# Kernel tuning notes

Measured on AMD Instinct MI355X. Metric: run time of the kernel, lower is better.

## Reference

```python
import jax, jax.numpy as jnp
import numpy as np

MAX_LENGTH = 400
NULL_TERM_IND = 52
THR = 1.0 - 1e-05  # F.threshold threshold value


def leaky(x):
    # F.leaky_relu default negative_slope=0.01
    return jnp.where(x >= 0, x, 0.01 * x)


def gru_cell(x, h, w_ih, w_hh, b_ih, b_hh):
    # torch.nn.GRUCell math
    gi = x @ w_ih.T + b_ih          # [B, 3H]
    gh = h @ w_hh.T + b_hh          # [B, 3H]
    i_r, i_z, i_n = jnp.split(gi, 3, axis=-1)
    h_r, h_z, h_n = jnp.split(gh, 3, axis=-1)
    r = jax.nn.sigmoid(i_r + h_r)
    z = jax.nn.sigmoid(i_z + h_z)
    n = jnp.tanh(i_n + r * h_n)
    return (1.0 - z) * n + z * h


def setup_inputs() -> dict:
    key = jax.random.key(0)
    ks = jax.random.split(key, 9)
    B, D, H, C = 2048, 4096, 128, 96
    def init(k, shape, fan):
        return (jax.random.uniform(k, shape, jnp.float32) * 2.0 - 1.0) / np.sqrt(fan)
    return {
        "img_feat": jax.random.normal(ks[0], (B, D), jnp.float32),
        "lin1_w": init(ks[1], (H, D), D),
        "lin1_b": init(ks[2], (H,), D),
        "w_ih": init(ks[3], (3 * H, H), H),
        "w_hh": init(ks[4], (3 * H, H), H),
        "b_ih": init(ks[5], (3 * H,), H),
        "b_hh": init(ks[6], (3 * H,), H),
        "lin2_w": init(ks[7], (C, H), H),
        "lin2_b": init(ks[8], (C,), H),
    }


def reference(img_feat, lin1_w, lin1_b, w_ih, w_hh, b_ih, b_hh, lin2_w, lin2_b):
    # ht: GRU input at t=0 is leaky_relu(lin1(img_feat)); hidden starts at zeros.
    ht = leaky(img_feat @ lin1_w.T + lin1_b)   # [B, 128]
    h0 = jnp.zeros_like(ht)

    def step(carry, _):
        ht, h0 = carry
        hn = gru_cell(ht, h0, w_ih, w_hh, b_ih, b_hh)
        # original: ht = char_gen(ht, h0); h0 = ht -> input == hidden next step
        chars = leaky(hn) @ lin2_w.T + lin2_b   # [B, C]
        m = jax.lax.stop_gradient(jnp.max(chars, axis=-1, keepdims=True))  # .data detach
        cn = chars / m
        cn = jnp.where(cn > THR, cn, 0.0)       # F.threshold(x, 1-1e-5, 0)
        return (hn, hn), cn

    _, titles = jax.lax.scan(step, (ht, h0), None, length=MAX_LENGTH)  # [T, B, C]
    titles = jnp.transpose(titles, (1, 0, 2))   # [B, T, C]

    # title_lens: first t with titles[b, t, NULL_TERM_IND] == 1, else MAX_LENGTH
    eq = titles[:, :, NULL_TERM_IND] == 1.0     # [B, T]
    first = jnp.argmax(eq, axis=1)
    lens = jnp.where(eq.any(axis=1), first + 1, MAX_LENGTH).astype(jnp.int32)
    return titles, lens
```

## Files before the change

kernel.cpp:

```cpp
#include <hip/hip_runtime.h>
#include <math.h>

#define NB   8
#define TT   400
#define HH   128
#define CC   96
#define DD   4096
#define THRV (1.0f - 1e-5f)
#define XR   40
#define HEPS 4e-6f
#define S10  1024.0f
#define IS10 0.0009765625f
#define IS20 9.5367431640625e-07f

typedef _Float16 f16x8 __attribute__((ext_vector_type(8)));
typedef float    f32x4 __attribute__((ext_vector_type(4)));
typedef float    f32x2 __attribute__((ext_vector_type(2)));
typedef int      i32x4 __attribute__((ext_vector_type(4)));
typedef unsigned long long ull;

__device__ __forceinline__ float rcp_fast(float x) {
#if __has_builtin(__builtin_amdgcn_rcpf)
    return __builtin_amdgcn_rcpf(x);
#else
    return 1.0f / x;
#endif
}
__device__ __forceinline__ float sigm(float v)  { return rcp_fast(1.0f + __expf(-v)); }
__device__ __forceinline__ float ftanh(float x) { return 1.0f - 2.0f * rcp_fast(1.0f + __expf(2.0f * x)); }

__device__ __forceinline__ void split2(float4 u0, float4 u1, f16x8& hi, f16x8& lo) {
    float x[8] = {u0.x, u0.y, u0.z, u0.w, u1.x, u1.y, u1.z, u1.w};
    #pragma unroll
    for (int e = 0; e < 8; ++e) {
        _Float16 h = (_Float16)x[e];
        hi[e] = h;
        lo[e] = (_Float16)(x[e] - (float)h);
    }
}
__device__ __forceinline__ void split2s(float4 u0, float4 u1, f16x8& hi, f16x8& lo) {
    float x[8] = {u0.x, u0.y, u0.z, u0.w, u1.x, u1.y, u1.z, u1.w};
    #pragma unroll
    for (int e = 0; e < 8; ++e) {
        _Float16 h = (_Float16)x[e];
        hi[e] = h;
        lo[e] = (_Float16)((x[e] - (float)h) * S10);
    }
}
__device__ __forceinline__ void split1(float x, _Float16& hi, _Float16& lo) {
    hi = (_Float16)x;
    lo = (_Float16)(x - (float)hi);
}

__device__ __forceinline__ float xsum32(float v) {
#if __has_builtin(__builtin_amdgcn_permlane32_swap)
    auto r = __builtin_amdgcn_permlane32_swap(__float_as_uint(v), __float_as_uint(v), false, false);
    return __uint_as_float(r[0]) + __uint_as_float(r[1]);
#else
    return v + __shfl_xor(v, 32, 64);
#endif
}

__device__ __forceinline__ void step_barrier() {
    __builtin_amdgcn_sched_barrier(0);
    asm volatile("s_waitcnt lgkmcnt(0)" ::: "memory");
    __builtin_amdgcn_s_barrier();
    asm volatile("" ::: "memory");
    __builtin_amdgcn_sched_barrier(0);
}

__global__ __launch_bounds__(1024, 4)
void gru_title(const float* __restrict__ img,
               const float* __restrict__ l1w,
               const float* __restrict__ l1b,
               const float* __restrict__ wih,
               const float* __restrict__ whh,
               const float* __restrict__ bih,
               const float* __restrict__ bhh,
               const float* __restrict__ l2w,
               const float* __restrict__ l2b,
               float* __restrict__ out,
               float* __restrict__ lens)
{
    __shared__ alignas(16) _Float16 x2 [2][64][XR];
    __shared__ alignas(16) _Float16 l2v[2][64][XR];
    __shared__ alignas(16) char     x2i8[2][64][32];
    __shared__ alignas(16) _Float16 bcS[2][6][4][4][16][8];
    __shared__ alignas(16) float    gEx[4096];
    __shared__ alignas(16) float    scr[2048];
    __shared__ alignas(16) float    xs0[NB][HH];
    __shared__ int sh_st[4];

    const int tid  = threadIdx.x;
    const int b0   = blockIdx.x * NB;
    const int w    = tid >> 6;
    const int lane = tid & 63;
    const int lm   = lane & 15;
    const int lq   = lane >> 4;
    const int c8   = w & 7;
    const int r8   = w >> 3;
    const int ic2  = 16 * c8 + lm;

    f16x8 bh[2][4];
    i32x4 bq[2][2];
    float gb[2], fq[2];
    #pragma unroll
    for (int gl = 0; gl < 2; ++gl) {
        const int g2 = 2 * r8 + gl;
        const float* r0;
        const float* r1 = nullptr;
        float bsum;
        if (g2 == 0)      { r0 = wih + (size_t)ic2 * HH;         r1 = whh + (size_t)ic2 * HH;         bsum = bih[ic2] + bhh[ic2]; }
        else if (g2 == 1) { r0 = wih + (size_t)(128 + ic2) * HH; r1 = whh + (size_t)(128 + ic2) * HH; bsum = bih[128 + ic2] + bhh[128 + ic2]; }
        else if (g2 == 2) { r0 = wih + (size_t)(256 + ic2) * HH;                                      bsum = bih[256 + ic2]; }
        else              { r0 = whh + (size_t)(256 + ic2) * HH;                                      bsum = bhh[256 + ic2]; }
        gb[gl] = bsum;
        float bl32[4][8];
        #pragma unroll
        for (int kt = 0; kt < 4; ++kt) {
            const int k0 = 32 * kt + 8 * lq;
            float4 u0 = *(const float4*)(r0 + k0);
            float4 u1 = *(const float4*)(r0 + k0 + 4);
            if (r1) {
                float4 e0 = *(const float4*)(r1 + k0);
                float4 e1 = *(const float4*)(r1 + k0 + 4);
                u0.x += e0.x; u0.y += e0.y; u0.z += e0.z; u0.w += e0.w;
                u1.x += e1.x; u1.y += e1.y; u1.z += e1.z; u1.w += e1.w;
            }
            float xv[8] = {u0.x, u0.y, u0.z, u0.w, u1.x, u1.y, u1.z, u1.w};
            f16x8 hiv;
            #pragma unroll
            for (int e = 0; e < 8; ++e) {
                _Float16 hh = (_Float16)xv[e];
                hiv[e] = hh;
                bl32[kt][e] = xv[e] - (float)hh;
            }
            bh[gl][kt] = hiv;
        }
        float mx = 0.f;
        #pragma unroll
        for (int kt = 0; kt < 4; ++kt)
            #pragma unroll
            for (int e = 0; e < 8; ++e) mx = fmaxf(mx, fabsf(bl32[kt][e]));
        mx = fmaxf(mx, __shfl_xor(mx, 16, 64));
        mx = fmaxf(mx, __shfl_xor(mx, 32, 64));
        const float inv = (mx > 0.f) ? 127.0f / mx : 0.f;
        fq[gl] = mx * (1.0f / 16129.0f);
        ull p[4];
        #pragma unroll
        for (int kt = 0; kt < 4; ++kt) {
            ull pv = 0;
            #pragma unroll
            for (int e = 0; e < 8; ++e) {
                int q = (int)rintf(bl32[kt][e] * inv);
                pv |= ((ull)((unsigned)q & 0xffu)) << (8 * e);
            }
            p[kt] = pv;
        }
        #pragma unroll
        for (int ktp = 0; ktp < 2; ++ktp) {
            ull s0a = __shfl(p[2 * ktp],     lm + 16 * ((2 * lq) & 3), 64);
            ull s0b = __shfl(p[2 * ktp + 1], lm + 16 * ((2 * lq) & 3), 64);
            ull lo8 = (lq & 2) ? s0b : s0a;
            ull s1a = __shfl(p[2 * ktp],     lm + 16 * ((2 * lq + 1) & 3), 64);
            ull s1b = __shfl(p[2 * ktp + 1], lm + 16 * ((2 * lq + 1) & 3), 64);
            ull hi8 = (lq & 2) ? s1b : s1a;
            i32x4 f;
            f[0] = (int)(unsigned)(lo8 & 0xffffffffu);
            f[1] = (int)(unsigned)(lo8 >> 32);
            f[2] = (int)(unsigned)(hi8 & 0xffffffffu);
            f[3] = (int)(unsigned)(hi8 >> 32);
            bq[gl][ktp] = f;
        }
    }

    const int ct = (w >= 1 && w <= 6) ? (w - 1) : -1;
    float cb = 0.f;
    if (ct >= 0) cb = l2b[16 * ct + lm];

    for (int idx = tid; idx < 6 * 4 * 4 * 16; idx += 1024) {
        int t_  = idx;
        int lm_ = t_ & 15; t_ >>= 4;
        int lq_ = t_ & 3;  t_ >>= 2;
        int kt_ = t_ & 3;  t_ >>= 2;
        int ct_ = t_;
        const int n  = 16 * ct_ + lm_;
        const int k0 = 32 * kt_ + 8 * lq_;
        #pragma unroll
        for (int e = 0; e < 8; ++e) {
            float v = l2w[(size_t)n * HH + k0 + e];
            _Float16 hi = (_Float16)v;
            bcS[0][ct_][kt_][lq_][lm_][e] = hi;
            bcS[1][ct_][kt_][lq_][lm_][e] = (_Float16)(v - (float)hi);
        }
    }

    if (tid < 4) sh_st[tid] = 1;
    ((int*)x2i8)[tid] = 0;

    {
        const int m8 = lm & 7;
        const float* arow = img + (size_t)(b0 + m8) * DD + 8 * lq + 2048 * r8;
        const float* brow = l1w + (size_t)ic2 * DD + 8 * lq + 2048 * r8;
        f32x4 z4 = {0.f, 0.f, 0.f, 0.f};
        f32x4 accP0 = z4, accP1 = z4, accQ0 = z4, accQ1 = z4;
        auto ptile = [&](int kt, f32x4& aP, f32x4& aQ) {
            float4 a0  = *(const float4*)(arow + 32 * kt);
            float4 a1  = *(const float4*)(arow + 32 * kt + 4);
            float4 bb0 = *(const float4*)(brow + 32 * kt);
            float4 bb1 = *(const float4*)(brow + 32 * kt + 4);
            f16x8 ah, al, bhf, blf;
            split2s(a0, a1, ah, al);
            split2s(bb0, bb1, bhf, blf);
            f16x8 af = (lm >= 8) ? al : ah;
            aP = __builtin_amdgcn_mfma_f32_16x16x32_f16(af, bhf, aP, 0, 0, 0);
            aQ = __builtin_amdgcn_mfma_f32_16x16x32_f16(af, blf, aQ, 0, 0, 0);
        };
        #pragma unroll 2
        for (int kt = 0; kt < 64; kt += 2) {
            ptile(kt,     accP0, accQ0);
            ptile(kt + 1, accP1, accQ1);
        }
        f32x4 P = accP0 + accP1;
        f32x4 Q = accQ0 + accQ1;
        const float sP = (lane < 32) ? 1.0f : IS10;
        const float sQ = (lane < 32) ? IS10 : IS20;
        float s0 = xsum32(P[0] * sP + Q[0] * sQ);
        float s1 = xsum32(P[1] * sP + Q[1] * sQ);
        float s2 = xsum32(P[2] * sP + Q[2] * sQ);
        float s3 = xsum32(P[3] * sP + Q[3] * sQ);
        if (lane < 32) {
            float vv[4] = {s0, s1, s2, s3};
            #pragma unroll
            for (int reg = 0; reg < 4; ++reg)
                scr[r8 * 1024 + (4 * lq + reg) * 128 + ic2] = vv[reg];
        }
    }
    __syncthreads();
    {
        const int m = tid >> 7, c = tid & 127;
        float v = scr[m * 128 + c] + scr[1024 + m * 128 + c] + l1b[c];
        xs0[m][c] = (v >= 0.f) ? v : 0.01f * v;
    }
    __syncthreads();

    const int mA = (lane < 32) ? 4 * lq : 4 * (lq - 2) + 2;

    const int mB  = w >> 1;
    const int iB  = 64 * (w & 1) + lane;
    const int rBq = 16 * ((iB >> 3) & 3);
    const int cBq = 8 * (iB >> 5) + (iB & 7);
    const int r8q = 16 * ((iB >> 4) & 3) + mB;
    const int c8q = 16 * (iB >> 6) + (iB & 15);
    const unsigned gRd = (unsigned)(mB * 2048 + iB * 16) ^ ((unsigned)(mB & 3) << 5);

    float hreg = 0.f;
    int  len   = TT;
    bool found = false;
    int  tex   = TT;

    auto chars_mfma = [&](int slot, f32x4& cA, f32x4& cB) {
        #pragma unroll
        for (int kt = 0; kt < 4; ++kt) {
            f16x8 cf = *(const f16x8*)&l2v[slot][lane][8 * kt];
            f16x8 bH = *(const f16x8*)&bcS[0][ct][kt][lq][lm][0];
            f16x8 bL = *(const f16x8*)&bcS[1][ct][kt][lq][lm][0];
            f32x4& a = (kt < 2) ? cA : cB;
            a = __builtin_amdgcn_mfma_f32_16x16x32_f16(cf, bH, a, 0, 0, 0);
            a = __builtin_amdgcn_mfma_f32_16x16x32_f16(cf, bL, a, 0, 0, 0);
        }
    };
    auto chars_commit = [&](int slot, f32x4 cA, f32x4 cB) {
        f32x4 ca = cA + cB;
        const int n = 16 * ct + lm;
        float s0 = xsum32(ca[0]);
        float s1 = xsum32(ca[1]);
        float s2 = xsum32(ca[2]);
        float s3 = xsum32(ca[3]);
        scr[slot * 1024 + mA * 128 + n]       = ((lane < 32) ? s0 : s2) + cb;
        scr[slot * 1024 + (mA + 1) * 128 + n] = ((lane < 32) ? s1 : s3) + cb;
    };

    auto outrow = [&](int slot, int tme, int r) {
        const float* cr = &scr[slot * 1024 + r * 128];
        float a0 = cr[lane];
        float a1 = cr[32 + lane];
        float a2 = cr[64 + lane];
        float mx = fmaxf(fmaxf(a0, a1), a2);
        mx = fmaxf(mx, __shfl_xor(mx, 16, 32));
        mx = fmaxf(mx, __shfl_xor(mx, 8, 32));
        mx = fmaxf(mx, __shfl_xor(mx, 4, 32));
        mx = fmaxf(mx, __shfl_xor(mx, 2, 32));
        mx = fmaxf(mx, __shfl_xor(mx, 1, 32));
        float q0 = a0 / mx;
        float q1 = a1 / mx;
        float q2 = a2 / mx;
        if (lane < 32) {
            size_t base = ((size_t)(b0 + r) * TT + tme) * CC;
            out[base + lane]      = (q0 > THRV) ? q0 : 0.f;
            out[base + 32 + lane] = (q1 > THRV) ? q1 : 0.f;
            out[base + 64 + lane] = (q2 > THRV) ? q2 : 0.f;
        }
        float q52 = __shfl(q1, 20, 64);
        if (!found && q52 == 1.0f) { found = true; len = tme + 1; }
    };

    for (int t = 0; t < TT; ++t) {
        const int pr = (t + 1) & 1;
        const int pc = t & 1;

        if (t == 0) {
            if (tid < 512) {
                const int g = tid >> 7;
                const int i = tid & 127;
                float bsum;
                if (g == 0)      bsum = bih[i] + bhh[i];
                else if (g == 1) bsum = bih[128 + i] + bhh[128 + i];
                else if (g == 2) bsum = bih[256 + i];
                else             bsum = bhh[256 + i];
                float accT[NB];
                #pragma unroll
                for (int m = 0; m < NB; ++m) accT[m] = bsum;
                if (g < 3) {
                    const float4* wp = (const float4*)(wih + (size_t)(128 * g + i) * HH);
                    #pragma unroll
                    for (int k = 0; k < HH / 4; ++k) {
                        float4 wv = wp[k];
                        #pragma unroll
                        for (int m = 0; m < NB; ++m) {
                            float4 x = *(const float4*)&xs0[m][4 * k];
                            accT[m] += wv.x * x.x + wv.y * x.y + wv.z * x.z + wv.w * x.w;
                        }
                    }
                }
                #pragma unroll
                for (int m = 0; m < NB; ++m) {
                    unsigned off = (unsigned)(m * 2048 + i * 16 + g * 4) ^ ((unsigned)(m & 3) << 5);
                    *(float*)((char*)gEx + off) = accT[m];
                }
            }
        } else {
            f32x4 z4 = {0.f, 0.f, 0.f, 0.f};
            i32x4 iz = {0, 0, 0, 0};
            if (ct >= 0) {
                f32x4 cc0 = z4, cc1 = z4;
                chars_mfma(pr, cc0, cc1);
                chars_commit(pr, cc0, cc1);
            }
            f32x4 acc[2] = {z4, z4};
            i32x4 qac[2] = {iz, iz};
            {
                f16x8 afA = *(const f16x8*)&x2[pr][lane][0];
                f16x8 afB = *(const f16x8*)&x2[pr][lane][8];
                acc[0] = __builtin_amdgcn_mfma_f32_16x16x32_f16(afA, bh[0][0], acc[0], 0, 0, 0);
                acc[1] = __builtin_amdgcn_mfma_f32_16x16x32_f16(afA, bh[1][0], acc[1], 0, 0, 0);
                acc[0] = __builtin_amdgcn_mfma_f32_16x16x32_f16(afB, bh[0][1], acc[0], 0, 0, 0);
                acc[1] = __builtin_amdgcn_mfma_f32_16x16x32_f16(afB, bh[1][1], acc[1], 0, 0, 0);
                afA = *(const f16x8*)&x2[pr][lane][16];
                afB = *(const f16x8*)&x2[pr][lane][24];
                acc[0] = __builtin_amdgcn_mfma_f32_16x16x32_f16(afA, bh[0][2], acc[0], 0, 0, 0);
                acc[1] = __builtin_amdgcn_mfma_f32_16x16x32_f16(afA, bh[1][2], acc[1], 0, 0, 0);
                acc[0] = __builtin_amdgcn_mfma_f32_16x16x32_f16(afB, bh[0][3], acc[0], 0, 0, 0);
                acc[1] = __builtin_amdgcn_mfma_f32_16x16x32_f16(afB, bh[1][3], acc[1], 0, 0, 0);
                i32x4 ia = *(const i32x4*)&x2i8[pr][lane][0];
                qac[0] = __builtin_amdgcn_mfma_i32_16x16x64_i8(ia, bq[0][0], qac[0], 0, 0, 0);
                qac[1] = __builtin_amdgcn_mfma_i32_16x16x64_i8(ia, bq[1][0], qac[1], 0, 0, 0);
                ia = *(const i32x4*)&x2i8[pr][lane][16];
                qac[0] = __builtin_amdgcn_mfma_i32_16x16x64_i8(ia, bq[0][1], qac[0], 0, 0, 0);
                qac[1] = __builtin_amdgcn_mfma_i32_16x16x64_i8(ia, bq[1][1], qac[1], 0, 0, 0);
            }
            float G[2][2];
            #pragma unroll
            for (int gl = 0; gl < 2; ++gl) {
                f32x4 t4;
                #pragma unroll
                for (int rr = 0; rr < 4; ++rr)
                    t4[rr] = acc[gl][rr] + fq[gl] * (float)qac[gl][rr];
                float c0 = xsum32(t4[0]);
                float c1 = xsum32(t4[1]);
                float c2 = xsum32(t4[2]);
                float c3 = xsum32(t4[3]);
                G[gl][0] = ((lane < 32) ? c0 : c2) + gb[gl];
                G[gl][1] = ((lane < 32) ? c1 : c3) + gb[gl];
            }
            #pragma unroll
            for (int s = 0; s < 2; ++s) {
                const int m = mA + s;
                unsigned off = (unsigned)(m * 2048 + ic2 * 16 + r8 * 8) ^ ((unsigned)(m & 3) << 5);
                f32x2 v2 = {G[0][s], G[1][s]};
                *(f32x2*)((char*)gEx + off) = v2;
            }
        }
        step_barrier();

        {
            float4 g4 = *(const float4*)((const char*)gEx + gRd);
            float r = sigm(g4.x);
            float z = sigm(g4.y);
            float n = ftanh(g4.z + r * g4.w);
            float hp = (t == 0) ? 0.f : hreg;
            float h  = (1.f - z) * n + z * hp;
            bool chg = (t < 2) | (fabsf(h - hp) > HEPS);
            hreg = h;
            float lv = (h >= 0.f) ? h : 0.01f * h;
            _Float16 a, b;
            split1(h, a, b);
            x2[pc][rBq + mB][cBq]     = a;
            x2[pc][rBq + 8 + mB][cBq] = b;
            split1(lv, a, b);
            l2v[pc][rBq + mB][cBq]     = a;
            l2v[pc][rBq + 8 + mB][cBq] = b;
            x2i8[pc][r8q][c8q] = (char)(int)rintf(h * 127.0f);
            if (chg) sh_st[t & 3] = 0;
        }
        if (w >= 8 && t >= 2) outrow(pc, t - 2, w - 8);
        if (tid == 0) sh_st[(t + 2) & 3] = 1;
        step_barrier();
        if (t >= 2 && sh_st[t & 3]) { tex = t; break; }
    }

    if (tex == TT) {
        const int pl = (TT - 1) & 1;
        if (ct >= 0) {
            f32x4 z4 = {0.f, 0.f, 0.f, 0.f};
            f32x4 cc0 = z4, cc1 = z4;
            chars_mfma(pl, cc0, cc1);
            chars_commit(pl, cc0, cc1);
        }
        if (w >= 8) outrow(TT & 1, TT - 2, w - 8);
        __syncthreads();
        if (w >= 8) outrow(pl, TT - 1, w - 8);
    } else if (w >= 8) {
        const int r = w - 8;
        outrow((tex + 1) & 1, tex - 1, r);
        size_t rowbase = (size_t)(b0 + r) * TT * CC;
        #pragma unroll
        for (int p = 0; p < 2; ++p) {
            const float* cr = &scr[p * 1024 + r * 128];
            float a0 = cr[lane];
            float a1 = cr[32 + lane];
            float a2 = cr[64 + lane];
            float mx = fmaxf(fmaxf(a0, a1), a2);
            mx = fmaxf(mx, __shfl_xor(mx, 16, 32));
            mx = fmaxf(mx, __shfl_xor(mx, 8, 32));
            mx = fmaxf(mx, __shfl_xor(mx, 4, 32));
            mx = fmaxf(mx, __shfl_xor(mx, 2, 32));
            mx = fmaxf(mx, __shfl_xor(mx, 1, 32));
            const int u0 = tex + (((tex & 1) == p) ? 0 : 1);
            if (lane < 32) {
                float q0 = a0 / mx;
                float q1 = a1 / mx;
                float q2 = a2 / mx;
                float w0v = (q0 > THRV) ? q0 : 0.f;
                float w1v = (q1 > THRV) ? q1 : 0.f;
                float w2v = (q2 > THRV) ? q2 : 0.f;
                for (int u = u0; u < TT; u += 2) {
                    out[rowbase + (size_t)u * CC + lane]      = w0v;
                    out[rowbase + (size_t)u * CC + 32 + lane] = w1v;
                    out[rowbase + (size_t)u * CC + 64 + lane] = w2v;
                }
            }
        }
    }

    if (w >= 8 && lane == 0) lens[b0 + (w - 8)] = (float)len;
}

extern "C" void kernel_launch(void* const* d_in, const int* in_sizes, int n_in,
                              void* d_out, int out_size, void* d_ws, size_t ws_size,
                              hipStream_t stream)
{
    const float* img = (const float*)d_in[0];
    const float* l1w = (const float*)d_in[1];
    const float* l1b = (const float*)d_in[2];
    const float* wih = (const float*)d_in[3];
    const float* whh = (const float*)d_in[4];
    const float* bih = (const float*)d_in[5];
    const float* bhh = (const float*)d_in[6];
    const float* l2w = (const float*)d_in[7];
    const float* l2b = (const float*)d_in[8];

    float* out  = (float*)d_out;
    float* lens = out + (size_t)2048 * TT * CC;

    gru_title<<<dim3(2048 / NB), dim3(1024), 0, stream>>>(
        img, l1w, l1b, wih, whh, bih, bhh, l2w, l2b, out, lens);
}
```

Measured before the change: 581.2 us.

## Pad and XOR-swizzle shared buffers, move output row write before step barrier

Pads the scratch rows from 128 to 132 floats and XOR-swizzles the column-block index of the x2/l2v fp16 fragments by quarter-lane group, so MFMA operand loads and hidden-state stores hit different LDS banks. It also moves the per-row output normalisation and store (outrow) from after the GRU update into the else-branch before the first step barrier, so it overlaps with gate-computing waves. The intent is to cut LDS bank conflicts and shorten the serial per-step critical path. The risk is a read-after-write race on the scr slot that outrow now reads in a different phase of the step.

```diff
diff --git a/kernel.cpp b/kernel.cpp
--- a/kernel.cpp
+++ b/kernel.cpp
@@ -12,6 +12,8 @@
 #define S10  1024.0f
 #define IS10 0.0009765625f
 #define IS20 9.5367431640625e-07f
+#define SCW  132
+#define SCS  1056
 
 typedef _Float16 f16x8 __attribute__((ext_vector_type(8)));
 typedef float    f32x4 __attribute__((ext_vector_type(4)));
@@ -87,7 +89,7 @@
     __shared__ alignas(16) char     x2i8[2][64][32];
     __shared__ alignas(16) _Float16 bcS[2][6][4][4][16][8];
     __shared__ alignas(16) float    gEx[4096];
-    __shared__ alignas(16) float    scr[2048];
+    __shared__ alignas(16) float    scr[2 * SCS];
     __shared__ alignas(16) float    xs0[NB][HH];
     __shared__ int sh_st[4];
 
@@ -233,13 +235,13 @@
             float vv[4] = {s0, s1, s2, s3};
             #pragma unroll
             for (int reg = 0; reg < 4; ++reg)
-                scr[r8 * 1024 + (4 * lq + reg) * 128 + ic2] = vv[reg];
+                scr[r8 * SCS + (4 * lq + reg) * SCW + ic2] = vv[reg];
         }
     }
     __syncthreads();
     {
         const int m = tid >> 7, c = tid & 127;
-        float v = scr[m * 128 + c] + scr[1024 + m * 128 + c] + l1b[c];
+        float v = scr[m * SCW + c] + scr[SCS + m * SCW + c] + l1b[c];
         xs0[m][c] = (v >= 0.f) ? v : 0.01f * v;
     }
     __syncthreads();
@@ -248,8 +250,9 @@
 
     const int mB  = w >> 1;
     const int iB  = 64 * (w & 1) + lane;
-    const int rBq = 16 * ((iB >> 3) & 3);
-    const int cBq = 8 * (iB >> 5) + (iB & 7);
+    const int kWr = (iB >> 3) & 3;
+    const int rBq = 16 * kWr;
+    const int cS  = 8 * (((iB >> 5) & 3) ^ kWr) + (iB & 7);
     const int r8q = 16 * ((iB >> 4) & 3) + mB;
     const int c8q = 16 * (iB >> 6) + (iB & 15);
     const unsigned gRd = (unsigned)(mB * 2048 + iB * 16) ^ ((unsigned)(mB & 3) << 5);
@@ -262,7 +265,7 @@
     auto chars_mfma = [&](int slot, f32x4& cA, f32x4& cB) {
         #pragma unroll
         for (int kt = 0; kt < 4; ++kt) {
-            f16x8 cf = *(const f16x8*)&l2v[slot][lane][8 * kt];
+            f16x8 cf = *(const f16x8*)&l2v[slot][lane][8 * (kt ^ lq)];
             f16x8 bH = *(const f16x8*)&bcS[0][ct][kt][lq][lm][0];
             f16x8 bL = *(const f16x8*)&bcS[1][ct][kt][lq][lm][0];
             f32x4& a = (kt < 2) ? cA : cB;
@@ -277,12 +280,12 @@
         float s1 = xsum32(ca[1]);
         float s2 = xsum32(ca[2]);
         float s3 = xsum32(ca[3]);
-        scr[slot * 1024 + mA * 128 + n]       = ((lane < 32) ? s0 : s2) + cb;
-        scr[slot * 1024 + (mA + 1) * 128 + n] = ((lane < 32) ? s1 : s3) + cb;
+        scr[slot * SCS + mA * SCW + n]       = ((lane < 32) ? s0 : s2) + cb;
+        scr[slot * SCS + (mA + 1) * SCW + n] = ((lane < 32) ? s1 : s3) + cb;
     };
 
     auto outrow = [&](int slot, int tme, int r) {
-        const float* cr = &scr[slot * 1024 + r * 128];
+        const float* cr = &scr[slot * SCS + r * SCW];
         float a0 = cr[lane];
         float a1 = cr[32 + lane];
         float a2 = cr[64 + lane];
@@ -350,14 +353,14 @@
             f32x4 acc[2] = {z4, z4};
             i32x4 qac[2] = {iz, iz};
             {
-                f16x8 afA = *(const f16x8*)&x2[pr][lane][0];
-                f16x8 afB = *(const f16x8*)&x2[pr][lane][8];
+                f16x8 afA = *(const f16x8*)&x2[pr][lane][8 * (0 ^ lq)];
+                f16x8 afB = *(const f16x8*)&x2[pr][lane][8 * (1 ^ lq)];
                 acc[0] = __builtin_amdgcn_mfma_f32_16x16x32_f16(afA, bh[0][0], acc[0], 0, 0, 0);
                 acc[1] = __builtin_amdgcn_mfma_f32_16x16x32_f16(afA, bh[1][0], acc[1], 0, 0, 0);
                 acc[0] = __builtin_amdgcn_mfma_f32_16x16x32_f16(afB, bh[0][1], acc[0], 0, 0, 0);
                 acc[1] = __builtin_amdgcn_mfma_f32_16x16x32_f16(afB, bh[1][1], acc[1], 0, 0, 0);
-                afA = *(const f16x8*)&x2[pr][lane][16];
-                afB = *(const f16x8*)&x2[pr][lane][24];
+                afA = *(const f16x8*)&x2[pr][lane][8 * (2 ^ lq)];
+                afB = *(const f16x8*)&x2[pr][lane][8 * (3 ^ lq)];
                 acc[0] = __builtin_amdgcn_mfma_f32_16x16x32_f16(afA, bh[0][2], acc[0], 0, 0, 0);
                 acc[1] = __builtin_amdgcn_mfma_f32_16x16x32_f16(afA, bh[1][2], acc[1], 0, 0, 0);
                 acc[0] = __builtin_amdgcn_mfma_f32_16x16x32_f16(afB, bh[0][3], acc[0], 0, 0, 0);
@@ -390,6 +393,7 @@
                 f32x2 v2 = {G[0][s], G[1][s]};
                 *(f32x2*)((char*)gEx + off) = v2;
             }
+            if (w >= 8 && t >= 2) outrow(pc, t - 2, w - 8);
         }
         step_barrier();
 
@@ -405,15 +409,14 @@
             float lv = (h >= 0.f) ? h : 0.01f * h;
             _Float16 a, b;
             split1(h, a, b);
-            x2[pc][rBq + mB][cBq]     = a;
-            x2[pc][rBq + 8 + mB][cBq] = b;
+            x2[pc][rBq + mB][cS]     = a;
+            x2[pc][rBq + 8 + mB][cS] = b;
             split1(lv, a, b);
-            l2v[pc][rBq + mB][cBq]     = a;
-            l2v[pc][rBq + 8 + mB][cBq] = b;
+            l2v[pc][rBq + mB][cS]     = a;
+            l2v[pc][rBq + 8 + mB][cS] = b;
             x2i8[pc][r8q][c8q] = (char)(int)rintf(h * 127.0f);
             if (chg) sh_st[t & 3] = 0;
         }
-        if (w >= 8 && t >= 2) outrow(pc, t - 2, w - 8);
         if (tid == 0) sh_st[(t + 2) & 3] = 1;
         step_barrier();
         if (t >= 2 && sh_st[t & 3]) { tex = t; break; }
@@ -436,7 +439,7 @@
         size_t rowbase = (size_t)(b0 + r) * TT * CC;
         #pragma unroll
         for (int p = 0; p < 2; ++p) {
-            const float* cr = &scr[p * 1024 + r * 128];
+            const float* cr = &scr[p * SCS + r * SCW];
             float a0 = cr[lane];
             float a1 = cr[32 + lane];
             float a2 = cr[64 + lane];
```

Measured after the change: 587.3 us. Within noise of the previous version (+1.1%).
